# Kernel optimization log

Hardware: AMD Instinct MI355X
Metric: run time of the kernel (lower is better)

## Reference

```python
import jax, jax.numpy as jnp
import numpy as np

N = 50000      # num nodes
E = 800000     # num edges (avg degree 16)
D_IN = 128     # input feature dim
H1 = 128       # hidden_dims[0]
H2 = 64        # hidden_dims[1]


def setup_inputs() -> dict:
    key = jax.random.key(0)
    ks = jax.random.split(key, 9)
    x = jax.random.normal(ks[0], (N, D_IN), dtype=jnp.float32)
    edge_index = jax.random.randint(ks[1], (2, E), 0, N, dtype=jnp.int32)
    def lin(k, d_in, d_out):
        s = 1.0 / np.sqrt(d_in)
        return jax.random.uniform(k, (d_in, d_out), jnp.float32, -s, s)
    # layer 1: lin_l (aggregated neighbors, has bias) and lin_r (root)
    Wl1 = lin(ks[2], D_IN, H1)
    bl1 = jnp.zeros((H1,), jnp.float32)
    Wr1 = lin(ks[3], D_IN, H1)
    # layer 2
    Wl2 = lin(ks[4], H1, H2)
    bl2 = jnp.zeros((H2,), jnp.float32)
    Wr2 = lin(ks[5], H1, H2)
    return {"x": x, "Wl1": Wl1, "bl1": bl1, "Wr1": Wr1,
            "Wl2": Wl2, "bl2": bl2, "Wr2": Wr2, "edge_index": edge_index}


def _sage_conv(x, src, dst, Wl, bl, Wr):
    # message = x[src] gathered per edge; mean-aggregate at dst
    msg = x[src]                                                   # [E, d_in]
    agg = jax.ops.segment_sum(msg, dst, num_segments=N)            # [N, d_in]
    deg = jax.ops.segment_sum(jnp.ones((src.shape[0],), x.dtype), dst,
                              num_segments=N)                      # [N]
    agg = agg / jnp.maximum(deg, 1.0)[:, None]
    # PyG SAGEConv: lin_l(agg) + lin_r(x_root), bias lives in lin_l
    return agg @ Wl + bl + x @ Wr


def reference(x, Wl1, bl1, Wr1, Wl2, bl2, Wr2, edge_index):
    src, dst = edge_index[0], edge_index[1]
    h = jax.nn.relu(_sage_conv(x, src, dst, Wl1, bl1, Wr1))        # [N, H1]
    # dropout p=0.0 (eval) -> identity
    return _sage_conv(h, src, dst, Wl2, bl2, Wr2)                  # [N, H2]
```

## Files before the change

kernel.cpp:

```cpp
#include <hip/hip_runtime.h>

#define D 128


__global__ __launch_bounds__(256) void hist_dst(
    const int* __restrict__ dst, int* __restrict__ cnt, int E)
{
    int e = blockIdx.x * blockDim.x + threadIdx.x;
    if (e < E) atomicAdd(&cnt[dst[e]], 1);
}

__global__ __launch_bounds__(256) void block_sum(
    const int* __restrict__ cnt, int* __restrict__ blk_sum, int n)
{
    __shared__ int s[256];
    int t = threadIdx.x;
    int i = blockIdx.x * 256 + t;
    s[t] = (i < n) ? cnt[i] : 0;
    __syncthreads();
    #pragma unroll
    for (int off = 128; off > 0; off >>= 1) {
        if (t < off) s[t] += s[t + off];
        __syncthreads();
    }
    if (t == 0) blk_sum[blockIdx.x] = s[0];
}

__global__ __launch_bounds__(256) void scan_blocks(
    const int* __restrict__ blk_sum, int* __restrict__ blk_off,
    int* __restrict__ row_ptr, int B, int n, int E)
{
    __shared__ int s[256];
    int t = threadIdx.x;
    int v = (t < B) ? blk_sum[t] : 0;
    s[t] = v;
    __syncthreads();
    #pragma unroll
    for (int off = 1; off < 256; off <<= 1) {
        int add = (t >= off) ? s[t - off] : 0;
        __syncthreads();
        s[t] += add;
        __syncthreads();
    }
    if (t < B) blk_off[t] = s[t] - v;
    if (t == 0) row_ptr[n] = E;
}

__global__ __launch_bounds__(256) void scan_final(
    const int* __restrict__ cnt, const int* __restrict__ blk_off,
    int* __restrict__ row_ptr, int* __restrict__ cursor, int n)
{
    __shared__ int s[256];
    int t = threadIdx.x;
    int i = blockIdx.x * 256 + t;
    int c = (i < n) ? cnt[i] : 0;
    s[t] = c;
    __syncthreads();
    #pragma unroll
    for (int off = 1; off < 256; off <<= 1) {
        int add = (t >= off) ? s[t - off] : 0;
        __syncthreads();
        s[t] += add;
        __syncthreads();
    }
    if (i < n) {
        int v = blk_off[blockIdx.x] + s[t] - c;
        row_ptr[i] = v;
        cursor[i] = v;
    }
}

__global__ __launch_bounds__(256) void fill_csr(
    const int* __restrict__ src, const int* __restrict__ dst,
    int* __restrict__ cursor, int* __restrict__ ebuf, int E)
{
    int e = blockIdx.x * blockDim.x + threadIdx.x;
    if (e >= E) return;
    int pos = atomicAdd(&cursor[dst[e]], 1);
    ebuf[pos] = src[e];
}


__global__ __launch_bounds__(256) void csr_mean_agg128(
    const float* __restrict__ feat, const int* __restrict__ row_ptr,
    const int* __restrict__ ebuf, float* __restrict__ agg, int n)
{
    int gid = blockIdx.x * blockDim.x + threadIdx.x;
    int node = gid >> 6;
    int lane = gid & 63;
    if (node >= n) return;
    int start = row_ptr[node];
    int end = row_ptr[node + 1];
    float ax = 0.0f, ay = 0.0f;
    for (int j0 = start; j0 < end; j0 += 64) {
        int m = min(64, end - j0);
        int myid = (lane < m) ? ebuf[j0 + lane] : 0;
        #pragma unroll 4
        for (int j = 0; j < m; ++j) {
            int s = __shfl(myid, j);
            float2 v = ((const float2*)(feat + (size_t)s * D))[lane];
            ax += v.x; ay += v.y;
        }
    }
    float inv = 1.0f / fmaxf((float)(end - start), 1.0f);
    ((float2*)(agg + (size_t)node * D))[lane] = make_float2(ax * inv, ay * inv);
}


__global__ __launch_bounds__(256) void sage_gemm1(
    const float* __restrict__ agg, const float* __restrict__ x,
    const float* __restrict__ Wl, const float* __restrict__ Wr,
    const float* __restrict__ bl, float* __restrict__ h, int n)
{
    __shared__ float As[128][33];
    __shared__ float Ws[32][132];
    const int tid = threadIdx.x;
    const int tx = tid & 15;
    const int ty = tid >> 4;
    const int row0 = blockIdx.x * 128;

    const int srow = tid >> 1;
    const int sseg = (tid & 1) * 16;
    const int wkk  = tid >> 3;
    const int wseg = (tid & 7) * 16;

    float acc[8][8];
    #pragma unroll
    for (int i = 0; i < 8; ++i)
        #pragma unroll
        for (int j = 0; j < 8; ++j) acc[i][j] = 0.0f;

    for (int c = 0; c < 8; ++c) {
        const float* Asrc = (c < 4) ? agg : x;
        const float* Wsrc = (c < 4) ? Wl : Wr;
        const int k0 = (c & 3) * 32;

        int gr = row0 + srow; if (gr >= n) gr = n - 1;
        const float4* ap = (const float4*)(Asrc + (size_t)gr * D + k0 + sseg);
        float4 a0 = ap[0], a1 = ap[1], a2 = ap[2], a3 = ap[3];
        const float4* wp = (const float4*)(Wsrc + (size_t)(k0 + wkk) * 128 + wseg);
        float4 w0 = wp[0], w1 = wp[1], w2 = wp[2], w3 = wp[3];

        __syncthreads();
        {
            float* ad = &As[srow][sseg];
            ad[0]=a0.x; ad[1]=a0.y; ad[2]=a0.z; ad[3]=a0.w;
            ad[4]=a1.x; ad[5]=a1.y; ad[6]=a1.z; ad[7]=a1.w;
            ad[8]=a2.x; ad[9]=a2.y; ad[10]=a2.z; ad[11]=a2.w;
            ad[12]=a3.x; ad[13]=a3.y; ad[14]=a3.z; ad[15]=a3.w;
            float* wd = &Ws[wkk][wseg];
            wd[0]=w0.x; wd[1]=w0.y; wd[2]=w0.z; wd[3]=w0.w;
            wd[4]=w1.x; wd[5]=w1.y; wd[6]=w1.z; wd[7]=w1.w;
            wd[8]=w2.x; wd[9]=w2.y; wd[10]=w2.z; wd[11]=w2.w;
            wd[12]=w3.x; wd[13]=w3.y; wd[14]=w3.z; wd[15]=w3.w;
        }
        __syncthreads();

        #pragma unroll 8
        for (int kk = 0; kk < 32; ++kk) {
            float av[8], wv[8];
            #pragma unroll
            for (int i = 0; i < 8; ++i) av[i] = As[ty * 8 + i][kk];
            #pragma unroll
            for (int j = 0; j < 8; ++j) wv[j] = Ws[kk][tx + 16 * j];
            #pragma unroll
            for (int i = 0; i < 8; ++i)
                #pragma unroll
                for (int j = 0; j < 8; ++j)
                    acc[i][j] = fmaf(av[i], wv[j], acc[i][j]);
        }
    }

    #pragma unroll
    for (int j = 0; j < 8; ++j) {
        float b = bl[tx + 16 * j];
        #pragma unroll
        for (int i = 0; i < 8; ++i) {
            int r = row0 + ty * 8 + i;
            if (r < n)
                h[(size_t)r * 128 + tx + 16 * j] = fmaxf(acc[i][j] + b, 0.0f);
        }
    }
}


__global__ __launch_bounds__(256) void sage_gemm2(
    const float* __restrict__ agg, const float* __restrict__ hin,
    const float* __restrict__ Wl, const float* __restrict__ Wr,
    const float* __restrict__ bl, float* __restrict__ out, int n)
{
    __shared__ float As[128][33];
    __shared__ float Ws[32][68];
    const int tid = threadIdx.x;
    const int tx = tid & 15;
    const int ty = tid >> 4;
    const int row0 = blockIdx.x * 128;

    const int srow = tid >> 1;
    const int sseg = (tid & 1) * 16;
    const int wkk  = tid >> 3;
    const int wseg = (tid & 7) * 8;

    float acc[8][4];
    #pragma unroll
    for (int i = 0; i < 8; ++i)
        #pragma unroll
        for (int j = 0; j < 4; ++j) acc[i][j] = 0.0f;

    for (int c = 0; c < 8; ++c) {
        const float* Asrc = (c < 4) ? agg : hin;
        const float* Wsrc = (c < 4) ? Wl : Wr;
        const int k0 = (c & 3) * 32;

        int gr = row0 + srow; if (gr >= n) gr = n - 1;
        const float4* ap = (const float4*)(Asrc + (size_t)gr * D + k0 + sseg);
        float4 a0 = ap[0], a1 = ap[1], a2 = ap[2], a3 = ap[3];
        const float4* wp = (const float4*)(Wsrc + (size_t)(k0 + wkk) * 64 + wseg);
        float4 w0 = wp[0], w1 = wp[1];

        __syncthreads();
        {
            float* ad = &As[srow][sseg];
            ad[0]=a0.x; ad[1]=a0.y; ad[2]=a0.z; ad[3]=a0.w;
            ad[4]=a1.x; ad[5]=a1.y; ad[6]=a1.z; ad[7]=a1.w;
            ad[8]=a2.x; ad[9]=a2.y; ad[10]=a2.z; ad[11]=a2.w;
            ad[12]=a3.x; ad[13]=a3.y; ad[14]=a3.z; ad[15]=a3.w;
            float* wd = &Ws[wkk][wseg];
            wd[0]=w0.x; wd[1]=w0.y; wd[2]=w0.z; wd[3]=w0.w;
            wd[4]=w1.x; wd[5]=w1.y; wd[6]=w1.z; wd[7]=w1.w;
        }
        __syncthreads();

        #pragma unroll 8
        for (int kk = 0; kk < 32; ++kk) {
            float av[8], wv[4];
            #pragma unroll
            for (int i = 0; i < 8; ++i) av[i] = As[ty * 8 + i][kk];
            #pragma unroll
            for (int j = 0; j < 4; ++j) wv[j] = Ws[kk][tx + 16 * j];
            #pragma unroll
            for (int i = 0; i < 8; ++i)
                #pragma unroll
                for (int j = 0; j < 4; ++j)
                    acc[i][j] = fmaf(av[i], wv[j], acc[i][j]);
        }
    }

    #pragma unroll
    for (int j = 0; j < 4; ++j) {
        float b = bl[tx + 16 * j];
        #pragma unroll
        for (int i = 0; i < 8; ++i) {
            int r = row0 + ty * 8 + i;
            if (r < n)
                out[(size_t)r * 64 + tx + 16 * j] = acc[i][j] + b;
        }
    }
}


extern "C" void kernel_launch(void* const* d_in, const int* in_sizes, int n_in,
                              void* d_out, int out_size, void* d_ws, size_t ws_size,
                              hipStream_t stream) {
    const float* x   = (const float*)d_in[0];
    const float* Wl1 = (const float*)d_in[1];
    const float* bl1 = (const float*)d_in[2];
    const float* Wr1 = (const float*)d_in[3];
    const float* Wl2 = (const float*)d_in[4];
    const float* bl2 = (const float*)d_in[5];
    const float* Wr2 = (const float*)d_in[6];
    const int*   ei  = (const int*)d_in[7];

    const int n = in_sizes[0] / D;
    const int E = in_sizes[7] / 2;
    const int* src = ei;
    const int* dst = ei + E;

    float* out = (float*)d_out;
    char* ws = (char*)d_ws;
    size_t off = 0;
    const size_t feat_bytes = (size_t)n * D * sizeof(float);
    float* agg     = (float*)(ws + off); off += feat_bytes;
    float* h       = (float*)(ws + off); off += feat_bytes;
    int*   row_ptr = (int*)(ws + off);   off += (size_t)(n + 1) * sizeof(int);
    int*   cursor  = (int*)(ws + off);   off += (size_t)n * sizeof(int);
    int*   cnt     = (int*)(ws + off);   off += (size_t)n * sizeof(int);
    int*   blk     = (int*)(ws + off);   off += 512 * sizeof(int);
    int*   ebuf    = (int*)(ws + off);   off += (size_t)E * sizeof(int);

    const int B = (n + 255) / 256;
    int* blk_sum = blk;
    int* blk_off = blk + 256;

    hipMemsetAsync(cnt, 0, (size_t)n * sizeof(int), stream);
    hist_dst<<<(E + 255) / 256, 256, 0, stream>>>(dst, cnt, E);
    block_sum<<<B, 256, 0, stream>>>(cnt, blk_sum, n);
    scan_blocks<<<1, 256, 0, stream>>>(blk_sum, blk_off, row_ptr, B, n, E);
    scan_final<<<B, 256, 0, stream>>>(cnt, blk_off, row_ptr, cursor, n);
    fill_csr<<<(E + 255) / 256, 256, 0, stream>>>(src, dst, cursor, ebuf, E);

    const int gemm_blocks = (n + 127) / 128;

    {
        long long total = (long long)n * 64;
        csr_mean_agg128<<<(int)((total + 255) / 256), 256, 0, stream>>>(
            x, row_ptr, ebuf, agg, n);
    }
    sage_gemm1<<<gemm_blocks, 256, 0, stream>>>(agg, x, Wl1, Wr1, bl1, h, n);

    {
        long long total = (long long)n * 64;
        csr_mean_agg128<<<(int)((total + 255) / 256), 256, 0, stream>>>(
            h, row_ptr, ebuf, agg, n);
    }
    sage_gemm2<<<gemm_blocks, 256, 0, stream>>>(agg, h, Wl2, Wr2, bl2, out, n);
}
```

Before: 408.4 us.

## Transform-then-aggregate with bf16 projected neighbor features

Moves the linear projection ahead of aggregation by linearity: each layer first computes x@Wl and x@Wr in one fused GEMM, then gathers the projected Wl features per edge and adds root, bias and ReLU inside the aggregation kernel. The gathered projection is stored as bf16, halving gather bytes, and in layer 2 the gather width drops from 128 to 64 columns. GEMM tiles are reshaped with XOR-swizzled shared-memory weight layout to avoid bank conflicts. Storing the gathered projection in bf16 loses precision relative to the fp32 reference.

```diff
diff --git a/kernel.cpp b/kernel.cpp
--- a/kernel.cpp
+++ b/kernel.cpp
@@ -1,6 +1,15 @@
 #include <hip/hip_runtime.h>
 
 #define D 128
+
+__device__ __forceinline__ float bf16_to_f32(unsigned short u) {
+    union { unsigned int i; float f; } c; c.i = ((unsigned int)u) << 16; return c.f;
+}
+__device__ __forceinline__ unsigned short f32_to_bf16(float f) {
+    union { float f; unsigned int i; } c; c.f = f;
+    unsigned int r = c.i + 0x7fffu + ((c.i >> 16) & 1u);
+    return (unsigned short)(r >> 16);
+}
 
 
 __global__ __launch_bounds__(256) void hist_dst(
@@ -81,9 +90,90 @@
 }
 
 
-__global__ __launch_bounds__(256) void csr_mean_agg128(
-    const float* __restrict__ feat, const int* __restrict__ row_ptr,
-    const int* __restrict__ ebuf, float* __restrict__ agg, int n)
+__global__ __launch_bounds__(256) void gemm_x(
+    const float* __restrict__ x, const float* __restrict__ Wl,
+    const float* __restrict__ Wr, unsigned short* __restrict__ Pl,
+    float* __restrict__ Pr, int n)
+{
+    __shared__ float As[64][33];
+    __shared__ float Ws[32][264];
+    const int tid = threadIdx.x;
+    const int tx = tid & 31;
+    const int ty = tid >> 5;
+    const int row0 = blockIdx.x * 64;
+
+    const int arow = tid >> 2;
+    const int aseg = (tid & 3) * 8;
+    const int wrow = tid >> 3;
+    const int wt   = tid & 7;
+    const float* wbase = (wt < 4) ? (Wl + wt * 32) : (Wr + (wt - 4) * 32);
+
+    float acc[8][8];
+    #pragma unroll
+    for (int i = 0; i < 8; ++i)
+        #pragma unroll
+        for (int j = 0; j < 8; ++j) acc[i][j] = 0.0f;
+
+    for (int c = 0; c < 4; ++c) {
+        const int k0 = c * 32;
+        int gr = row0 + arow; if (gr >= n) gr = n - 1;
+        const float4* ap = (const float4*)(x + (size_t)gr * D + k0 + aseg);
+        float4 a0 = ap[0], a1 = ap[1];
+        const float4* wp = (const float4*)(wbase + (size_t)(k0 + wrow) * D);
+        float4 wrg[8];
+        #pragma unroll
+        for (int q = 0; q < 8; ++q) wrg[q] = wp[q];
+
+        __syncthreads();
+        {
+            float* ad = &As[arow][aseg];
+            ad[0]=a0.x; ad[1]=a0.y; ad[2]=a0.z; ad[3]=a0.w;
+            ad[4]=a1.x; ad[5]=a1.y; ad[6]=a1.z; ad[7]=a1.w;
+            float* wd = &Ws[wrow][wt * 32];
+            #pragma unroll
+            for (int q = 0; q < 8; ++q) {
+                wd[(4*q+0) ^ wt] = wrg[q].x;
+                wd[(4*q+1) ^ wt] = wrg[q].y;
+                wd[(4*q+2) ^ wt] = wrg[q].z;
+                wd[(4*q+3) ^ wt] = wrg[q].w;
+            }
+        }
+        __syncthreads();
+
+        #pragma unroll 4
+        for (int kk = 0; kk < 32; ++kk) {
+            float av[8], wv[8];
+            #pragma unroll
+            for (int i = 0; i < 8; ++i) av[i] = As[ty * 8 + i][kk];
+            #pragma unroll
+            for (int j = 0; j < 8; ++j) wv[j] = Ws[kk][32 * j + (tx ^ j)];
+            #pragma unroll
+            for (int i = 0; i < 8; ++i)
+                #pragma unroll
+                for (int j = 0; j < 8; ++j)
+                    acc[i][j] = fmaf(av[i], wv[j], acc[i][j]);
+        }
+    }
+
+    #pragma unroll
+    for (int i = 0; i < 8; ++i) {
+        int r = row0 + ty * 8 + i;
+        if (r < n) {
+            #pragma unroll
+            for (int j = 0; j < 4; ++j)
+                Pl[(size_t)r * 128 + tx + 32 * j] = f32_to_bf16(acc[i][j]);
+            #pragma unroll
+            for (int j = 0; j < 4; ++j)
+                Pr[(size_t)r * 128 + tx + 32 * j] = acc[i][4 + j];
+        }
+    }
+}
+
+
+__global__ __launch_bounds__(256) void agg_relu1(
+    const unsigned short* __restrict__ Pl, const float* __restrict__ Pr,
+    const float* __restrict__ b, const int* __restrict__ row_ptr,
+    const int* __restrict__ ebuf, float* __restrict__ h, int n)
 {
     int gid = blockIdx.x * blockDim.x + threadIdx.x;
     int node = gid >> 6;
@@ -98,108 +188,38 @@
         #pragma unroll 4
         for (int j = 0; j < m; ++j) {
             int s = __shfl(myid, j);
-            float2 v = ((const float2*)(feat + (size_t)s * D))[lane];
-            ax += v.x; ay += v.y;
+            unsigned int v = *(const unsigned int*)(Pl + (size_t)s * 128 + 2 * lane);
+            ax += bf16_to_f32((unsigned short)(v & 0xffff));
+            ay += bf16_to_f32((unsigned short)(v >> 16));
         }
     }
     float inv = 1.0f / fmaxf((float)(end - start), 1.0f);
-    ((float2*)(agg + (size_t)node * D))[lane] = make_float2(ax * inv, ay * inv);
-}
-
-
-__global__ __launch_bounds__(256) void sage_gemm1(
-    const float* __restrict__ agg, const float* __restrict__ x,
-    const float* __restrict__ Wl, const float* __restrict__ Wr,
-    const float* __restrict__ bl, float* __restrict__ h, int n)
-{
-    __shared__ float As[128][33];
-    __shared__ float Ws[32][132];
+    float2 pr = *(const float2*)(Pr + (size_t)node * 128 + 2 * lane);
+    float2 bb = *(const float2*)(b + 2 * lane);
+    float2 o;
+    o.x = fmaxf(ax * inv + pr.x + bb.x, 0.0f);
+    o.y = fmaxf(ay * inv + pr.y + bb.y, 0.0f);
+    *(float2*)(h + (size_t)node * 128 + 2 * lane) = o;
+}
+
+
+__global__ __launch_bounds__(256) void gemm_h(
+    const float* __restrict__ hin, const float* __restrict__ Wl,
+    const float* __restrict__ Wr, unsigned short* __restrict__ Ql,
+    float* __restrict__ Qr, int n)
+{
+    __shared__ float As[64][33];
+    __shared__ float Ws[32][136];
     const int tid = threadIdx.x;
-    const int tx = tid & 15;
-    const int ty = tid >> 4;
-    const int row0 = blockIdx.x * 128;
-
-    const int srow = tid >> 1;
-    const int sseg = (tid & 1) * 16;
-    const int wkk  = tid >> 3;
-    const int wseg = (tid & 7) * 16;
-
-    float acc[8][8];
-    #pragma unroll
-    for (int i = 0; i < 8; ++i)
-        #pragma unroll
-        for (int j = 0; j < 8; ++j) acc[i][j] = 0.0f;
-
-    for (int c = 0; c < 8; ++c) {
-        const float* Asrc = (c < 4) ? agg : x;
-        const float* Wsrc = (c < 4) ? Wl : Wr;
-        const int k0 = (c & 3) * 32;
-
-        int gr = row0 + srow; if (gr >= n) gr = n - 1;
-        const float4* ap = (const float4*)(Asrc + (size_t)gr * D + k0 + sseg);
-        float4 a0 = ap[0], a1 = ap[1], a2 = ap[2], a3 = ap[3];
-        const float4* wp = (const float4*)(Wsrc + (size_t)(k0 + wkk) * 128 + wseg);
-        float4 w0 = wp[0], w1 = wp[1], w2 = wp[2], w3 = wp[3];
-
-        __syncthreads();
-        {
-            float* ad = &As[srow][sseg];
-            ad[0]=a0.x; ad[1]=a0.y; ad[2]=a0.z; ad[3]=a0.w;
-            ad[4]=a1.x; ad[5]=a1.y; ad[6]=a1.z; ad[7]=a1.w;
-            ad[8]=a2.x; ad[9]=a2.y; ad[10]=a2.z; ad[11]=a2.w;
-            ad[12]=a3.x; ad[13]=a3.y; ad[14]=a3.z; ad[15]=a3.w;
-            float* wd = &Ws[wkk][wseg];
-            wd[0]=w0.x; wd[1]=w0.y; wd[2]=w0.z; wd[3]=w0.w;
-            wd[4]=w1.x; wd[5]=w1.y; wd[6]=w1.z; wd[7]=w1.w;
-            wd[8]=w2.x; wd[9]=w2.y; wd[10]=w2.z; wd[11]=w2.w;
-            wd[12]=w3.x; wd[13]=w3.y; wd[14]=w3.z; wd[15]=w3.w;
-        }
-        __syncthreads();
-
-        #pragma unroll 8
-        for (int kk = 0; kk < 32; ++kk) {
-            float av[8], wv[8];
-            #pragma unroll
-            for (int i = 0; i < 8; ++i) av[i] = As[ty * 8 + i][kk];
-            #pragma unroll
-            for (int j = 0; j < 8; ++j) wv[j] = Ws[kk][tx + 16 * j];
-            #pragma unroll
-            for (int i = 0; i < 8; ++i)
-                #pragma unroll
-                for (int j = 0; j < 8; ++j)
-                    acc[i][j] = fmaf(av[i], wv[j], acc[i][j]);
-        }
-    }
-
-    #pragma unroll
-    for (int j = 0; j < 8; ++j) {
-        float b = bl[tx + 16 * j];
-        #pragma unroll
-        for (int i = 0; i < 8; ++i) {
-            int r = row0 + ty * 8 + i;
-            if (r < n)
-                h[(size_t)r * 128 + tx + 16 * j] = fmaxf(acc[i][j] + b, 0.0f);
-        }
-    }
-}
-
-
-__global__ __launch_bounds__(256) void sage_gemm2(
-    const float* __restrict__ agg, const float* __restrict__ hin,
-    const float* __restrict__ Wl, const float* __restrict__ Wr,
-    const float* __restrict__ bl, float* __restrict__ out, int n)
-{
-    __shared__ float As[128][33];
-    __shared__ float Ws[32][68];
-    const int tid = threadIdx.x;
-    const int tx = tid & 15;
-    const int ty = tid >> 4;
-    const int row0 = blockIdx.x * 128;
-
-    const int srow = tid >> 1;
-    const int sseg = (tid & 1) * 16;
-    const int wkk  = tid >> 3;
-    const int wseg = (tid & 7) * 8;
+    const int tx = tid & 31;
+    const int ty = tid >> 5;
+    const int row0 = blockIdx.x * 64;
+
+    const int arow = tid >> 2;
+    const int aseg = (tid & 3) * 8;
+    const int wrow = tid >> 3;
+    const int wt   = tid & 7;
+    const float* wbase = (wt < 4) ? (Wl + wt * 16) : (Wr + (wt - 4) * 16);
 
     float acc[8][4];
     #pragma unroll
@@ -207,37 +227,42 @@
         #pragma unroll
         for (int j = 0; j < 4; ++j) acc[i][j] = 0.0f;
 
-    for (int c = 0; c < 8; ++c) {
-        const float* Asrc = (c < 4) ? agg : hin;
-        const float* Wsrc = (c < 4) ? Wl : Wr;
-        const int k0 = (c & 3) * 32;
-
-        int gr = row0 + srow; if (gr >= n) gr = n - 1;
-        const float4* ap = (const float4*)(Asrc + (size_t)gr * D + k0 + sseg);
-        float4 a0 = ap[0], a1 = ap[1], a2 = ap[2], a3 = ap[3];
-        const float4* wp = (const float4*)(Wsrc + (size_t)(k0 + wkk) * 64 + wseg);
-        float4 w0 = wp[0], w1 = wp[1];
+    for (int c = 0; c < 4; ++c) {
+        const int k0 = c * 32;
+        int gr = row0 + arow; if (gr >= n) gr = n - 1;
+        const float4* ap = (const float4*)(hin + (size_t)gr * D + k0 + aseg);
+        float4 a0 = ap[0], a1 = ap[1];
+        const float4* wp = (const float4*)(wbase + (size_t)(k0 + wrow) * 64);
+        float4 wrg[4];
+        #pragma unroll
+        for (int q = 0; q < 4; ++q) wrg[q] = wp[q];
 
         __syncthreads();
         {
-            float* ad = &As[srow][sseg];
+            float* ad = &As[arow][aseg];
             ad[0]=a0.x; ad[1]=a0.y; ad[2]=a0.z; ad[3]=a0.w;
             ad[4]=a1.x; ad[5]=a1.y; ad[6]=a1.z; ad[7]=a1.w;
-            ad[8]=a2.x; ad[9]=a2.y; ad[10]=a2.z; ad[11]=a2.w;
-            ad[12]=a3.x; ad[13]=a3.y; ad[14]=a3.z; ad[15]=a3.w;
-            float* wd = &Ws[wkk][wseg];
-            wd[0]=w0.x; wd[1]=w0.y; wd[2]=w0.z; wd[3]=w0.w;
-            wd[4]=w1.x; wd[5]=w1.y; wd[6]=w1.z; wd[7]=w1.w;
-        }
-        __syncthreads();
-
-        #pragma unroll 8
+            float* wd = &Ws[wrow][wt * 16];
+            #pragma unroll
+            for (int q = 0; q < 4; ++q) {
+                wd[(4*q+0) ^ wt] = wrg[q].x;
+                wd[(4*q+1) ^ wt] = wrg[q].y;
+                wd[(4*q+2) ^ wt] = wrg[q].z;
+                wd[(4*q+3) ^ wt] = wrg[q].w;
+            }
+        }
+        __syncthreads();
+
+        #pragma unroll 4
         for (int kk = 0; kk < 32; ++kk) {
             float av[8], wv[4];
             #pragma unroll
             for (int i = 0; i < 8; ++i) av[i] = As[ty * 8 + i][kk];
             #pragma unroll
-            for (int j = 0; j < 4; ++j) wv[j] = Ws[kk][tx + 16 * j];
+            for (int j = 0; j < 4; ++j) {
+                int g = 2 * j + (tx >> 4);
+                wv[j] = Ws[kk][16 * g + ((tx & 15) ^ g)];
+            }
             #pragma unroll
             for (int i = 0; i < 8; ++i)
                 #pragma unroll
@@ -247,15 +272,43 @@
     }
 
     #pragma unroll
-    for (int j = 0; j < 4; ++j) {
-        float b = bl[tx + 16 * j];
-        #pragma unroll
-        for (int i = 0; i < 8; ++i) {
-            int r = row0 + ty * 8 + i;
-            if (r < n)
-                out[(size_t)r * 64 + tx + 16 * j] = acc[i][j] + b;
-        }
-    }
+    for (int i = 0; i < 8; ++i) {
+        int r = row0 + ty * 8 + i;
+        if (r < n) {
+            #pragma unroll
+            for (int j = 0; j < 2; ++j)
+                Ql[(size_t)r * 64 + tx + 32 * j] = f32_to_bf16(acc[i][j]);
+            #pragma unroll
+            for (int j = 0; j < 2; ++j)
+                Qr[(size_t)r * 64 + tx + 32 * j] = acc[i][2 + j];
+        }
+    }
+}
+
+
+__global__ __launch_bounds__(256) void agg2(
+    const unsigned short* __restrict__ Ql, const float* __restrict__ Qr,
+    const float* __restrict__ b, const int* __restrict__ row_ptr,
+    const int* __restrict__ ebuf, float* __restrict__ out, int n)
+{
+    int gid = blockIdx.x * blockDim.x + threadIdx.x;
+    int node = gid >> 6;
+    int lane = gid & 63;
+    if (node >= n) return;
+    int start = row_ptr[node];
+    int end = row_ptr[node + 1];
+    float ax = 0.0f;
+    for (int j0 = start; j0 < end; j0 += 64) {
+        int m = min(64, end - j0);
+        int myid = (lane < m) ? ebuf[j0 + lane] : 0;
+        #pragma unroll 4
+        for (int j = 0; j < m; ++j) {
+            int s = __shfl(myid, j);
+            ax += bf16_to_f32(Ql[(size_t)s * 64 + lane]);
+        }
+    }
+    float inv = 1.0f / fmaxf((float)(end - start), 1.0f);
+    out[(size_t)node * 64 + lane] = ax * inv + Qr[(size_t)node * 64 + lane] + b[lane];
 }
 
 
@@ -279,14 +332,17 @@
     float* out = (float*)d_out;
     char* ws = (char*)d_ws;
     size_t off = 0;
-    const size_t feat_bytes = (size_t)n * D * sizeof(float);
-    float* agg     = (float*)(ws + off); off += feat_bytes;
-    float* h       = (float*)(ws + off); off += feat_bytes;
-    int*   row_ptr = (int*)(ws + off);   off += (size_t)(n + 1) * sizeof(int);
-    int*   cursor  = (int*)(ws + off);   off += (size_t)n * sizeof(int);
-    int*   cnt     = (int*)(ws + off);   off += (size_t)n * sizeof(int);
-    int*   blk     = (int*)(ws + off);   off += 512 * sizeof(int);
-    int*   ebuf    = (int*)(ws + off);   off += (size_t)E * sizeof(int);
+    unsigned short* Pl = (unsigned short*)(ws + off); off += (size_t)n * 128 * 2;
+    float* Pr = (float*)(ws + off); off += (size_t)n * 128 * 4;
+    float* h  = (float*)(ws + off); off += (size_t)n * 128 * 4;
+    int* row_ptr = (int*)(ws + off); off += (size_t)(n + 1) * 4;
+    int* cursor  = (int*)(ws + off); off += (size_t)n * 4;
+    int* cnt     = (int*)(ws + off); off += (size_t)n * 4;
+    int* blk     = (int*)(ws + off); off += 512 * 4;
+    int* ebuf    = (int*)(ws + off); off += (size_t)E * 4;
+
+    unsigned short* Ql = Pl;
+    float* Qr = Pr;
 
     const int B = (n + 255) / 256;
     int* blk_sum = blk;
@@ -299,19 +355,12 @@
     scan_final<<<B, 256, 0, stream>>>(cnt, blk_off, row_ptr, cursor, n);
     fill_csr<<<(E + 255) / 256, 256, 0, stream>>>(src, dst, cursor, ebuf, E);
 
-    const int gemm_blocks = (n + 127) / 128;
-
-    {
-        long long total = (long long)n * 64;
-        csr_mean_agg128<<<(int)((total + 255) / 256), 256, 0, stream>>>(
-            x, row_ptr, ebuf, agg, n);
-    }
-    sage_gemm1<<<gemm_blocks, 256, 0, stream>>>(agg, x, Wl1, Wr1, bl1, h, n);
-
-    {
-        long long total = (long long)n * 64;
-        csr_mean_agg128<<<(int)((total + 255) / 256), 256, 0, stream>>>(
-            h, row_ptr, ebuf, agg, n);
-    }
-    sage_gemm2<<<gemm_blocks, 256, 0, stream>>>(agg, h, Wl2, Wr2, bl2, out, n);
-}
+    const int gblocks = (n + 63) / 64;
+    const int ablocks = (int)(((long long)n * 64 + 255) / 256);
+
+    gemm_x<<<gblocks, 256, 0, stream>>>(x, Wl1, Wr1, Pl, Pr, n);
+    agg_relu1<<<ablocks, 256, 0, stream>>>(Pl, Pr, bl1, row_ptr, ebuf, h, n);
+
+    gemm_h<<<gblocks, 256, 0, stream>>>(h, Wl2, Wr2, Ql, Qr, n);
+    agg2<<<ablocks, 256, 0, stream>>>(Ql, Qr, bl2, row_ptr, ebuf, out, n);
+}
```

Measured after the change: 374.0 us. 1.09x faster.
